# Optimization experiments

Hardware: AMD Instinct MI355X
Metric: run time of the kernel (lower is better)

## Reference

```python
import jax, jax.numpy as jnp
import numpy as np

HIDDEN = 1024
HEADS = 16
D_K = HIDDEN // HEADS
B, S = 2, 2048


def setup_inputs() -> dict:
    key = jax.random.key(0)
    ks = jax.random.split(key, 11)
    sc = 1.0 / np.sqrt(HIDDEN)
    return {
        "query": jax.random.normal(ks[0], (B, S, HIDDEN), jnp.float32),
        "key": jax.random.normal(ks[1], (B, S, HIDDEN), jnp.float32),
        "value": jax.random.normal(ks[2], (B, S, HIDDEN), jnp.float32),
        "w_q": jax.random.normal(ks[3], (HIDDEN, HIDDEN), jnp.float32) * sc,
        "b_q": jax.random.normal(ks[4], (HIDDEN,), jnp.float32) * 0.02,
        "w_k": jax.random.normal(ks[5], (HIDDEN, HIDDEN), jnp.float32) * sc,
        "b_k": jax.random.normal(ks[6], (HIDDEN,), jnp.float32) * 0.02,
        "w_v": jax.random.normal(ks[7], (HIDDEN, HIDDEN), jnp.float32) * sc,
        "b_v": jax.random.normal(ks[8], (HIDDEN,), jnp.float32) * 0.02,
        "w_o": jax.random.normal(ks[9], (HIDDEN, HIDDEN), jnp.float32) * sc,
        "b_o": jax.random.normal(ks[10], (HIDDEN,), jnp.float32) * 0.02,
    }


def reference(query, key, value, w_q, b_q, w_k, b_k, w_v, b_v, w_o, b_o):
    b, s, _ = query.shape
    # linear projections (torch Linear: x @ W^T + b)
    q = query @ w_q.T + b_q
    k = key @ w_k.T + b_k
    v = value @ w_v.T + b_v
    # [B, H, S, D]
    q = q.reshape(b, s, HEADS, D_K).transpose(0, 2, 1, 3)
    k = k.reshape(b, s, HEADS, D_K).transpose(0, 2, 1, 3)
    v = v.reshape(b, s, HEADS, D_K).transpose(0, 2, 1, 3)
    scale = jnp.float32(1.0 / np.sqrt(D_K))
    scores = jnp.einsum('bhqd,bhkd->bhqk', q, k) * scale  # [B,H,S,S]
    probs = jax.nn.softmax(scores, axis=-1)
    y = jnp.einsum('bhqk,bhkd->bhqd', probs, v)
    y = y.transpose(0, 2, 1, 3).reshape(b, s, HIDDEN)
    return y @ w_o.T + b_o
```

## Files before the change

kernel.cpp:

```cpp
#include <hip/hip_runtime.h>
#include <hip/hip_bf16.h>
#include <math.h>

#define HIDDEN 1024
#define HEADS 16
#define DK 64
#define BB 2
#define SS 2048
#define MROWS (BB*SS)

typedef __attribute__((ext_vector_type(8))) short short8;
typedef __attribute__((ext_vector_type(4))) float f32x4;
typedef __attribute__((ext_vector_type(16))) float f32x16;
typedef __attribute__((ext_vector_type(4))) unsigned short ushort4_t;

static __device__ __forceinline__ unsigned short f2bf(float f) {
    unsigned int u = __float_as_uint(f);
    u += 0x7fffu + ((u >> 16) & 1u);
    return (unsigned short)(u >> 16);
}

static __device__ __forceinline__ unsigned int cvtpk(float lo, float hi) {
    unsigned int r;
    asm volatile("v_cvt_pk_bf16_f32 %0, %1, %2" : "=v"(r) : "v"(lo), "v"(hi));
    return r;
}
static __device__ __forceinline__ void swap32(unsigned int& a, unsigned int& b) {
    asm volatile("v_permlane32_swap_b32 %0, %1" : "+v"(a), "+v"(b));
}

__global__ __launch_bounds__(256) void cast_all(
    const float* __restrict__ q, const float* __restrict__ k, const float* __restrict__ v,
    const float* __restrict__ wq, const float* __restrict__ wk, const float* __restrict__ wv,
    unsigned short* __restrict__ Xq, unsigned short* __restrict__ Xk, unsigned short* __restrict__ Xv,
    unsigned short* __restrict__ Wq, unsigned short* __restrict__ Wk, unsigned short* __restrict__ Wv) {
    int i = blockIdx.x * 256 + threadIdx.x;
    const float* src; unsigned short* dst; int off;
    if (i < (3 << 20)) {
        int w = i >> 20; off = i & ((1 << 20) - 1);
        src = (w == 0) ? q : (w == 1) ? k : v;
        dst = (w == 0) ? Xq : (w == 1) ? Xk : Xv;
    } else {
        int j = i - (3 << 20);
        int w = j >> 18; off = j & ((1 << 18) - 1);
        src = (w == 0) ? wq : (w == 1) ? wk : wv;
        dst = (w == 0) ? Wq : (w == 1) ? Wk : Wv;
    }
    float4 f = reinterpret_cast<const float4*>(src)[off];
    ushort4_t o;
    o.x = f2bf(f.x); o.y = f2bf(f.y); o.z = f2bf(f.z); o.w = f2bf(f.w);
    reinterpret_cast<ushort4_t*>(dst)[off] = o;
}

__global__ __launch_bounds__(256, 3) void gemm_qkv(
    const unsigned short* __restrict__ Xq, const unsigned short* __restrict__ Xk, const unsigned short* __restrict__ Xv,
    const unsigned short* __restrict__ Wq, const unsigned short* __restrict__ Wk, const unsigned short* __restrict__ Wv,
    const float* __restrict__ bq, const float* __restrict__ bk, const float* __restrict__ bv,
    unsigned short* __restrict__ Qb, unsigned short* __restrict__ Kb, unsigned short* __restrict__ Vt,
    float scale_q) {
    __shared__ unsigned short As[128][40];
    __shared__ unsigned short Bs[128][40];
    const int lid = blockIdx.x + 8 * (blockIdx.y + 32 * blockIdx.z);
    const int c = lid & 7, i2 = lid >> 3;
    const int nb = i2 & 7;
    const int band = c * 12 + (i2 >> 3);
    const int yb = band & 31;
    const int z  = band >> 5;
    const unsigned short* A  = (z == 0) ? Xq : (z == 1) ? Xk : Xv;
    const unsigned short* Wt = (z == 0) ? Wq : (z == 1) ? Wk : Wv;
    const float* bias = (z == 0) ? bq : (z == 1) ? bk : bv;
    unsigned short* O = (z == 0) ? Qb : (z == 1) ? Kb : Vt;
    const float oscale = (z == 0) ? scale_q : 1.0f;

    const int t    = threadIdx.x;
    const int lane = t & 63;
    const int wave = t >> 6;
    const int m0 = yb * 128;
    const int n0 = nb * 128;
    const int row  = t >> 2;
    const int col8 = (t & 3) * 8;

    const int wm = (wave >> 1) * 64;
    const int wn = (wave & 1) * 64;
    const int lr = lane & 15;
    const int lk = (lane >> 4) * 8;

    f32x4 acc[4][4];
#pragma unroll
    for (int i = 0; i < 4; i++)
#pragma unroll
        for (int j = 0; j < 4; j++) acc[i][j] = f32x4{0.f, 0.f, 0.f, 0.f};

    for (int k0 = 0; k0 < HIDDEN; k0 += 32) {
        short8 av0 = *reinterpret_cast<const short8*>(A  + (size_t)(m0 + row)      * HIDDEN + k0 + col8);
        short8 av1 = *reinterpret_cast<const short8*>(A  + (size_t)(m0 + row + 64) * HIDDEN + k0 + col8);
        short8 bv0 = *reinterpret_cast<const short8*>(Wt + (size_t)(n0 + row)      * HIDDEN + k0 + col8);
        short8 bv1 = *reinterpret_cast<const short8*>(Wt + (size_t)(n0 + row + 64) * HIDDEN + k0 + col8);
        __syncthreads();
        *reinterpret_cast<short8*>(&As[row][col8])      = av0;
        *reinterpret_cast<short8*>(&As[row + 64][col8]) = av1;
        *reinterpret_cast<short8*>(&Bs[row][col8])      = bv0;
        *reinterpret_cast<short8*>(&Bs[row + 64][col8]) = bv1;
        __syncthreads();
        short8 af[4], bfr[4];
#pragma unroll
        for (int i = 0; i < 4; i++) af[i]  = *reinterpret_cast<const short8*>(&As[wm + i * 16 + lr][lk]);
#pragma unroll
        for (int j = 0; j < 4; j++) bfr[j] = *reinterpret_cast<const short8*>(&Bs[wn + j * 16 + lr][lk]);
#pragma unroll
        for (int i = 0; i < 4; i++)
#pragma unroll
            for (int j = 0; j < 4; j++)
                acc[i][j] = __builtin_amdgcn_mfma_f32_16x16x32_bf16(af[i], bfr[j], acc[i][j], 0, 0, 0);
    }

#pragma unroll
    for (int i = 0; i < 4; i++) {
        int mrow = m0 + wm + i * 16 + (lane >> 4) * 4;
#pragma unroll
        for (int j = 0; j < 4; j++) {
            int ncol = n0 + wn + j * 16 + lr;
            float bvv = bias[ncol];
            int b_ = mrow >> 11;
            int h_ = ncol >> 6;
            int d_ = ncol & 63;
            if (z != 2) {
#pragma unroll
                for (int r = 0; r < 4; r++) {
                    int s_ = (mrow + r) & 2047;
                    O[(((size_t)(b_ * HEADS + h_)) * SS + s_) * DK + d_] = f2bf((acc[i][j][r] + bvv) * oscale);
                }
            } else {
                int s0 = mrow & 2047;
                ushort4_t pk;
                pk.x = f2bf(acc[i][j][0] + bvv);
                pk.y = f2bf(acc[i][j][1] + bvv);
                pk.z = f2bf(acc[i][j][2] + bvv);
                pk.w = f2bf(acc[i][j][3] + bvv);
                *reinterpret_cast<ushort4_t*>(O + (((size_t)(b_ * HEADS + h_) * DK + d_) * SS + s0)) = pk;
            }
        }
    }
}

__global__ __launch_bounds__(256) void gemm_o(const unsigned short* __restrict__ A,
                                              const float* __restrict__ Wt,
                                              const float* __restrict__ bias,
                                              float* __restrict__ O) {
    __shared__ unsigned short As[128][40];
    __shared__ unsigned short Bs[64][40];
    const int lid = blockIdx.x + 16 * blockIdx.y;
    const int c = lid & 7, i2 = lid >> 3;
    const int nb = i2 & 15;
    const int band = c * 4 + (i2 >> 4);
    const int t    = threadIdx.x;
    const int lane = t & 63;
    const int wave = t >> 6;
    const int m0 = band * 128;
    const int n0 = nb * 64;
    const int row  = t >> 2;
    const int col8 = (t & 3) * 8;

    const int wm = wave * 32;
    const int lr = lane & 15;
    const int lk = (lane >> 4) * 8;

    f32x4 acc[2][4];
#pragma unroll
    for (int i = 0; i < 2; i++)
#pragma unroll
        for (int j = 0; j < 4; j++) acc[i][j] = f32x4{0.f, 0.f, 0.f, 0.f};

    for (int k0 = 0; k0 < HIDDEN; k0 += 32) {
        short8 av0 = *reinterpret_cast<const short8*>(A + (size_t)(m0 + row)      * HIDDEN + k0 + col8);
        short8 av1 = *reinterpret_cast<const short8*>(A + (size_t)(m0 + row + 64) * HIDDEN + k0 + col8);
        const float* w0 = Wt + (size_t)(n0 + row) * HIDDEN + k0 + col8;
        float4 w00 = reinterpret_cast<const float4*>(w0)[0];
        float4 w01 = reinterpret_cast<const float4*>(w0)[1];
        __syncthreads();
        *reinterpret_cast<short8*>(&As[row][col8])      = av0;
        *reinterpret_cast<short8*>(&As[row + 64][col8]) = av1;
        {
            union { unsigned int u[4]; short8 s; } pk;
            pk.u[0] = cvtpk(w00.x, w00.y);
            pk.u[1] = cvtpk(w00.z, w00.w);
            pk.u[2] = cvtpk(w01.x, w01.y);
            pk.u[3] = cvtpk(w01.z, w01.w);
            *reinterpret_cast<short8*>(&Bs[row][col8]) = pk.s;
        }
        __syncthreads();
        short8 af[2], bfr[4];
#pragma unroll
        for (int i = 0; i < 2; i++) af[i]  = *reinterpret_cast<const short8*>(&As[wm + i * 16 + lr][lk]);
#pragma unroll
        for (int j = 0; j < 4; j++) bfr[j] = *reinterpret_cast<const short8*>(&Bs[j * 16 + lr][lk]);
#pragma unroll
        for (int i = 0; i < 2; i++)
#pragma unroll
            for (int j = 0; j < 4; j++)
                acc[i][j] = __builtin_amdgcn_mfma_f32_16x16x32_bf16(af[i], bfr[j], acc[i][j], 0, 0, 0);
    }

#pragma unroll
    for (int i = 0; i < 2; i++) {
        int mrow = m0 + wm + i * 16 + (lane >> 4) * 4;
#pragma unroll
        for (int j = 0; j < 4; j++) {
            int ncol = n0 + j * 16 + lr;
            float bvv = bias[ncol];
#pragma unroll
            for (int r = 0; r < 4; r++)
                O[(size_t)(mrow + r) * HIDDEN + ncol] = acc[i][j][r] + bvv;
        }
    }
}

__global__ __launch_bounds__(256, 2) void attn_kernel(const unsigned short* __restrict__ Qb,
                                                      const unsigned short* __restrict__ Kb,
                                                      const unsigned short* __restrict__ Vt,
                                                      unsigned short* __restrict__ Yb) {
    __shared__ __attribute__((aligned(16))) unsigned short Ksh[2][64 * 64];
    __shared__ __attribute__((aligned(16))) unsigned short Vsh[2][64 * 64];
    __shared__ float Lsh[4][32];

    const int t    = threadIdx.x;
    const int lane = t & 63;
    const int wave = t >> 6;
    const int fid  = blockIdx.x;
    const int qblk = (fid >> 3) & 15;
    const int bh   = (fid & 7) * 4 + (fid >> 7);
    const int b_ = bh >> 4, h_ = bh & 15;
    const int qbase = qblk * 128 + wave * 32;
    const unsigned short* Qp = Qb + (size_t)bh * SS * DK;
    const unsigned short* Kp = Kb + (size_t)bh * SS * DK;
    const unsigned short* Vp = Vt + (size_t)bh * DK * SS;
    const int lq = lane & 31;
    const int hi = lane >> 5;
    const int sr = lane >> 3;
    const int cs = (lane & 7) ^ sr;

    short8 qf[4];
#pragma unroll
    for (int c = 0; c < 4; c++)
        qf[c] = *reinterpret_cast<const short8*>(Qp + (size_t)(qbase + lq) * DK + c * 16 + hi * 8);

    f32x16 acc0 = {0.f}, acc1 = {0.f};
#pragma unroll
    for (int r = 0; r < 16; r++) { acc0[r] = 0.f; acc1[r] = 0.f; }
    float mi = -INFINITY, li = 0.f;

#define STAGE(BUF, KV0) do {                                                                 \
    __builtin_amdgcn_global_load_lds(                                                        \
        (const __attribute__((address_space(1))) unsigned int*)(Kp + (size_t)((KV0) + wave * 16 + sr) * DK + cs * 8), \
        (__attribute__((address_space(3))) unsigned int*)&Ksh[BUF][(wave * 16) * 64], 16, 0, 0); \
    __builtin_amdgcn_global_load_lds(                                                        \
        (const __attribute__((address_space(1))) unsigned int*)(Kp + (size_t)((KV0) + wave * 16 + 8 + sr) * DK + cs * 8), \
        (__attribute__((address_space(3))) unsigned int*)&Ksh[BUF][(wave * 16 + 8) * 64], 16, 0, 0); \
    __builtin_amdgcn_global_load_lds(                                                        \
        (const __attribute__((address_space(1))) unsigned int*)(Vp + (size_t)(wave * 16 + sr) * SS + (KV0) + cs * 8), \
        (__attribute__((address_space(3))) unsigned int*)&Vsh[BUF][(wave * 16) * 64], 16, 0, 0); \
    __builtin_amdgcn_global_load_lds(                                                        \
        (const __attribute__((address_space(1))) unsigned int*)(Vp + (size_t)(wave * 16 + 8 + sr) * SS + (KV0) + cs * 8), \
        (__attribute__((address_space(3))) unsigned int*)&Vsh[BUF][(wave * 16 + 8) * 64], 16, 0, 0); \
} while (0)

    STAGE(0, 0);
    __syncthreads();

    for (int kv0 = 0; kv0 < SS; kv0 += 64) {
        const int cur = (kv0 >> 6) & 1;
        if (kv0 + 64 < SS) STAGE(cur ^ 1, kv0 + 64);

        f32x16 sv0, sv1;
#pragma unroll
        for (int r = 0; r < 16; r++) { sv0[r] = 0.f; sv1[r] = 0.f; }
#pragma unroll
        for (int c = 0; c < 4; c++) {
            short8 kf0 = *reinterpret_cast<const short8*>(
                &Ksh[cur][lq * 64 + (((2 * c + hi) ^ (lq & 7)) << 3)]);
            short8 kf1 = *reinterpret_cast<const short8*>(
                &Ksh[cur][(32 + lq) * 64 + (((2 * c + hi) ^ (lq & 7)) << 3)]);
            sv0 = __builtin_amdgcn_mfma_f32_32x32x16_bf16(kf0, qf[c], sv0, 0, 0, 0);
            sv1 = __builtin_amdgcn_mfma_f32_32x32x16_bf16(kf1, qf[c], sv1, 0, 0, 0);
        }

        float vmax = sv0[0];
#pragma unroll
        for (int r = 0; r < 16; r++) { vmax = fmaxf(vmax, sv0[r]); vmax = fmaxf(vmax, sv1[r]); }
        vmax = fmaxf(vmax, __shfl_xor(vmax, 32));
        if (!__all(vmax <= mi + 8.0f)) {
            float mnew = fmaxf(mi, vmax);
            float sc = __builtin_amdgcn_exp2f(mi - mnew);
            li *= sc;
            acc0 = acc0 * sc;
            acc1 = acc1 * sc;
            mi = mnew;
        }
        float pt[2][16];
        float rs = 0.f;
#pragma unroll
        for (int r = 0; r < 16; r++) {
            pt[0][r] = __builtin_amdgcn_exp2f(sv0[r] - mi);
            pt[1][r] = __builtin_amdgcn_exp2f(sv1[r] - mi);
            rs += pt[0][r] + pt[1][r];
        }
        rs += __shfl_xor(rs, 32);
        li += rs;

        short8 fragP[4];
#pragma unroll
        for (int tt = 0; tt < 2; tt++)
#pragma unroll
            for (int cl = 0; cl < 2; cl++) {
                unsigned int w0 = cvtpk(pt[tt][cl * 8 + 0], pt[tt][cl * 8 + 1]);
                unsigned int w1 = cvtpk(pt[tt][cl * 8 + 2], pt[tt][cl * 8 + 3]);
                unsigned int w2 = cvtpk(pt[tt][cl * 8 + 4], pt[tt][cl * 8 + 5]);
                unsigned int w3 = cvtpk(pt[tt][cl * 8 + 6], pt[tt][cl * 8 + 7]);
                swap32(w0, w2);
                swap32(w1, w3);
                union { unsigned int u[4]; short8 s; } f;
                f.u[0] = w0; f.u[1] = w1; f.u[2] = w2; f.u[3] = w3;
                fragP[tt * 2 + cl] = f.s;
            }

#pragma unroll
        for (int cc = 0; cc < 4; cc++) {
            short8 vf0 = *reinterpret_cast<const short8*>(
                &Vsh[cur][lq * 64 + (((2 * cc + hi) ^ (lq & 7)) << 3)]);
            short8 vf1 = *reinterpret_cast<const short8*>(
                &Vsh[cur][(32 + lq) * 64 + (((2 * cc + hi) ^ (lq & 7)) << 3)]);
            acc0 = __builtin_amdgcn_mfma_f32_32x32x16_bf16(fragP[cc], vf0, acc0, 0, 0, 0);
            acc1 = __builtin_amdgcn_mfma_f32_32x32x16_bf16(fragP[cc], vf1, acc1, 0, 0, 0);
        }
        __syncthreads();
    }
#undef STAGE

    if (lane < 32) Lsh[wave][lq] = 1.0f / li;
    __syncthreads();
#pragma unroll
    for (int r = 0; r < 16; r++) {
        int qr = (r & 3) + 8 * (r >> 2) + 4 * hi;
        float inv = Lsh[wave][qr];
        size_t base = ((size_t)b_ * SS + qbase + qr) * HIDDEN + h_ * 64 + lq;
        Yb[base]      = f2bf(acc0[r] * inv);
        Yb[base + 32] = f2bf(acc1[r] * inv);
    }
}

extern "C" void kernel_launch(void* const* d_in, const int* in_sizes, int n_in,
                              void* d_out, int out_size, void* d_ws, size_t ws_size,
                              hipStream_t stream) {
    const float* query = (const float*)d_in[0];
    const float* key_  = (const float*)d_in[1];
    const float* value = (const float*)d_in[2];
    const float* w_q = (const float*)d_in[3];
    const float* b_q = (const float*)d_in[4];
    const float* w_k = (const float*)d_in[5];
    const float* b_k = (const float*)d_in[6];
    const float* w_v = (const float*)d_in[7];
    const float* b_v = (const float*)d_in[8];
    const float* w_o = (const float*)d_in[9];
    const float* b_o = (const float*)d_in[10];

    const size_t SZ_X = (size_t)MROWS * HIDDEN * 2;
    const size_t SZ_W = (size_t)HIDDEN * HIDDEN * 2;
    char* ws = (char*)d_ws;
    unsigned short* Xq = (unsigned short*)(ws);
    unsigned short* Xk = (unsigned short*)(ws + SZ_X);
    unsigned short* Xv = (unsigned short*)(ws + 2 * SZ_X);
    unsigned short* Wq = (unsigned short*)(ws + 3 * SZ_X);
    unsigned short* Wk = (unsigned short*)(ws + 3 * SZ_X + SZ_W);
    unsigned short* Wv = (unsigned short*)(ws + 3 * SZ_X + 2 * SZ_W);
    unsigned short* Qb  = (unsigned short*)(ws + 3 * SZ_X + 3 * SZ_W);
    unsigned short* Kbf = (unsigned short*)(ws + 4 * SZ_X + 3 * SZ_W);
    unsigned short* Vt  = (unsigned short*)(ws + 5 * SZ_X + 3 * SZ_W);
    unsigned short* Yb  = (unsigned short*)(ws + 6 * SZ_X + 3 * SZ_W);

    cast_all<<<15360, 256, 0, stream>>>(query, key_, value, w_q, w_k, w_v,
                                        Xq, Xk, Xv, Wq, Wk, Wv);

    const float SCALE_Q = 0.125f * 1.4426950408889634f;
    gemm_qkv<<<dim3(8, 32, 3), 256, 0, stream>>>(
        Xq, Xk, Xv, Wq, Wk, Wv, b_q, b_k, b_v, Qb, Kbf, Vt, SCALE_Q);

    attn_kernel<<<dim3(512), 256, 0, stream>>>(Qb, Kbf, Vt, Yb);

    gemm_o<<<dim3(16, 32), 256, 0, stream>>>(Yb, w_o, b_o, (float*)d_out);
}
```

Baseline: 132.3 us.

## Fuse fp32 casts into QKV GEMM and split attention KV into two halves

```diff
diff --git a/kernel.cpp b/kernel.cpp
--- a/kernel.cpp
+++ b/kernel.cpp
@@ -19,6 +19,9 @@
     u += 0x7fffu + ((u >> 16) & 1u);
     return (unsigned short)(u >> 16);
 }
+static __device__ __forceinline__ float bf2f(unsigned short s) {
+    return __uint_as_float(((unsigned int)s) << 16);
+}
 
 static __device__ __forceinline__ unsigned int cvtpk(float lo, float hi) {
     unsigned int r;
@@ -28,33 +31,18 @@
 static __device__ __forceinline__ void swap32(unsigned int& a, unsigned int& b) {
     asm volatile("v_permlane32_swap_b32 %0, %1" : "+v"(a), "+v"(b));
 }
-
-__global__ __launch_bounds__(256) void cast_all(
-    const float* __restrict__ q, const float* __restrict__ k, const float* __restrict__ v,
-    const float* __restrict__ wq, const float* __restrict__ wk, const float* __restrict__ wv,
-    unsigned short* __restrict__ Xq, unsigned short* __restrict__ Xk, unsigned short* __restrict__ Xv,
-    unsigned short* __restrict__ Wq, unsigned short* __restrict__ Wk, unsigned short* __restrict__ Wv) {
-    int i = blockIdx.x * 256 + threadIdx.x;
-    const float* src; unsigned short* dst; int off;
-    if (i < (3 << 20)) {
-        int w = i >> 20; off = i & ((1 << 20) - 1);
-        src = (w == 0) ? q : (w == 1) ? k : v;
-        dst = (w == 0) ? Xq : (w == 1) ? Xk : Xv;
-    } else {
-        int j = i - (3 << 20);
-        int w = j >> 18; off = j & ((1 << 18) - 1);
-        src = (w == 0) ? wq : (w == 1) ? wk : wv;
-        dst = (w == 0) ? Wq : (w == 1) ? Wk : Wv;
-    }
-    float4 f = reinterpret_cast<const float4*>(src)[off];
-    ushort4_t o;
-    o.x = f2bf(f.x); o.y = f2bf(f.y); o.z = f2bf(f.z); o.w = f2bf(f.w);
-    reinterpret_cast<ushort4_t*>(dst)[off] = o;
+static __device__ __forceinline__ short8 pack_bf16x8(float4 lo, float4 hi) {
+    union { unsigned int u[4]; short8 s; } r;
+    r.u[0] = cvtpk(lo.x, lo.y);
+    r.u[1] = cvtpk(lo.z, lo.w);
+    r.u[2] = cvtpk(hi.x, hi.y);
+    r.u[3] = cvtpk(hi.z, hi.w);
+    return r.s;
 }
 
 __global__ __launch_bounds__(256, 3) void gemm_qkv(
-    const unsigned short* __restrict__ Xq, const unsigned short* __restrict__ Xk, const unsigned short* __restrict__ Xv,
-    const unsigned short* __restrict__ Wq, const unsigned short* __restrict__ Wk, const unsigned short* __restrict__ Wv,
+    const float* __restrict__ Xq, const float* __restrict__ Xk, const float* __restrict__ Xv,
+    const float* __restrict__ Wq, const float* __restrict__ Wk, const float* __restrict__ Wv,
     const float* __restrict__ bq, const float* __restrict__ bk, const float* __restrict__ bv,
     unsigned short* __restrict__ Qb, unsigned short* __restrict__ Kb, unsigned short* __restrict__ Vt,
     float scale_q) {
@@ -66,8 +54,8 @@
     const int band = c * 12 + (i2 >> 3);
     const int yb = band & 31;
     const int z  = band >> 5;
-    const unsigned short* A  = (z == 0) ? Xq : (z == 1) ? Xk : Xv;
-    const unsigned short* Wt = (z == 0) ? Wq : (z == 1) ? Wk : Wv;
+    const float* A  = (z == 0) ? Xq : (z == 1) ? Xk : Xv;
+    const float* Wt = (z == 0) ? Wq : (z == 1) ? Wk : Wv;
     const float* bias = (z == 0) ? bq : (z == 1) ? bk : bv;
     unsigned short* O = (z == 0) ? Qb : (z == 1) ? Kb : Vt;
     const float oscale = (z == 0) ? scale_q : 1.0f;
@@ -92,15 +80,23 @@
         for (int j = 0; j < 4; j++) acc[i][j] = f32x4{0.f, 0.f, 0.f, 0.f};
 
     for (int k0 = 0; k0 < HIDDEN; k0 += 32) {
-        short8 av0 = *reinterpret_cast<const short8*>(A  + (size_t)(m0 + row)      * HIDDEN + k0 + col8);
-        short8 av1 = *reinterpret_cast<const short8*>(A  + (size_t)(m0 + row + 64) * HIDDEN + k0 + col8);
-        short8 bv0 = *reinterpret_cast<const short8*>(Wt + (size_t)(n0 + row)      * HIDDEN + k0 + col8);
-        short8 bv1 = *reinterpret_cast<const short8*>(Wt + (size_t)(n0 + row + 64) * HIDDEN + k0 + col8);
+        const float* a0 = A  + (size_t)(m0 + row)      * HIDDEN + k0 + col8;
+        const float* a1 = A  + (size_t)(m0 + row + 64) * HIDDEN + k0 + col8;
+        const float* w0 = Wt + (size_t)(n0 + row)      * HIDDEN + k0 + col8;
+        const float* w1 = Wt + (size_t)(n0 + row + 64) * HIDDEN + k0 + col8;
+        float4 a00 = reinterpret_cast<const float4*>(a0)[0];
+        float4 a01 = reinterpret_cast<const float4*>(a0)[1];
+        float4 a10 = reinterpret_cast<const float4*>(a1)[0];
+        float4 a11 = reinterpret_cast<const float4*>(a1)[1];
+        float4 w00 = reinterpret_cast<const float4*>(w0)[0];
+        float4 w01 = reinterpret_cast<const float4*>(w0)[1];
+        float4 w10 = reinterpret_cast<const float4*>(w1)[0];
+        float4 w11 = reinterpret_cast<const float4*>(w1)[1];
         __syncthreads();
-        *reinterpret_cast<short8*>(&As[row][col8])      = av0;
-        *reinterpret_cast<short8*>(&As[row + 64][col8]) = av1;
-        *reinterpret_cast<short8*>(&Bs[row][col8])      = bv0;
-        *reinterpret_cast<short8*>(&Bs[row + 64][col8]) = bv1;
+        *reinterpret_cast<short8*>(&As[row][col8])      = pack_bf16x8(a00, a01);
+        *reinterpret_cast<short8*>(&As[row + 64][col8]) = pack_bf16x8(a10, a11);
+        *reinterpret_cast<short8*>(&Bs[row][col8])      = pack_bf16x8(w00, w01);
+        *reinterpret_cast<short8*>(&Bs[row + 64][col8]) = pack_bf16x8(w10, w11);
         __syncthreads();
         short8 af[4], bfr[4];
 #pragma unroll
@@ -180,14 +176,7 @@
         __syncthreads();
         *reinterpret_cast<short8*>(&As[row][col8])      = av0;
         *reinterpret_cast<short8*>(&As[row + 64][col8]) = av1;
-        {
-            union { unsigned int u[4]; short8 s; } pk;
-            pk.u[0] = cvtpk(w00.x, w00.y);
-            pk.u[1] = cvtpk(w00.z, w00.w);
-            pk.u[2] = cvtpk(w01.x, w01.y);
-            pk.u[3] = cvtpk(w01.z, w01.w);
-            *reinterpret_cast<short8*>(&Bs[row][col8]) = pk.s;
-        }
+        *reinterpret_cast<short8*>(&Bs[row][col8])      = pack_bf16x8(w00, w01);
         __syncthreads();
         short8 af[2], bfr[4];
 #pragma unroll
@@ -215,10 +204,12 @@
     }
 }
 
-__global__ __launch_bounds__(256, 2) void attn_kernel(const unsigned short* __restrict__ Qb,
+__global__ __launch_bounds__(256, 4) void attn_kernel(const unsigned short* __restrict__ Qb,
                                                       const unsigned short* __restrict__ Kb,
                                                       const unsigned short* __restrict__ Vt,
-                                                      unsigned short* __restrict__ Yb) {
+                                                      unsigned short* __restrict__ Yb0,
+                                                      unsigned short* __restrict__ Yb1,
+                                                      float2* __restrict__ ml) {
     __shared__ __attribute__((aligned(16))) unsigned short Ksh[2][64 * 64];
     __shared__ __attribute__((aligned(16))) unsigned short Vsh[2][64 * 64];
     __shared__ float Lsh[4][32];
@@ -227,10 +218,15 @@
     const int lane = t & 63;
     const int wave = t >> 6;
     const int fid  = blockIdx.x;
-    const int qblk = (fid >> 3) & 15;
-    const int bh   = (fid & 7) * 4 + (fid >> 7);
+    const int c    = fid & 7;
+    const int i    = fid >> 3;
+    const int qblk = i & 15;
+    const int pair = c * 8 + (i >> 4);
+    const int bh   = pair >> 1;
+    const int kvh  = pair & 1;
     const int b_ = bh >> 4, h_ = bh & 15;
     const int qbase = qblk * 128 + wave * 32;
+    const int kvbase = kvh << 10;
     const unsigned short* Qp = Qb + (size_t)bh * SS * DK;
     const unsigned short* Kp = Kb + (size_t)bh * SS * DK;
     const unsigned short* Vp = Vt + (size_t)bh * DK * SS;
@@ -241,10 +237,10 @@
 
     short8 qf[4];
 #pragma unroll
-    for (int c = 0; c < 4; c++)
-        qf[c] = *reinterpret_cast<const short8*>(Qp + (size_t)(qbase + lq) * DK + c * 16 + hi * 8);
-
-    f32x16 acc0 = {0.f}, acc1 = {0.f};
+    for (int cc = 0; cc < 4; cc++)
+        qf[cc] = *reinterpret_cast<const short8*>(Qp + (size_t)(qbase + lq) * DK + cc * 16 + hi * 8);
+
+    f32x16 acc0, acc1;
 #pragma unroll
     for (int r = 0; r < 16; r++) { acc0[r] = 0.f; acc1[r] = 0.f; }
     float mi = -INFINITY, li = 0.f;
@@ -264,24 +260,24 @@
         (__attribute__((address_space(3))) unsigned int*)&Vsh[BUF][(wave * 16 + 8) * 64], 16, 0, 0); \
 } while (0)
 
-    STAGE(0, 0);
+    STAGE(0, kvbase);
     __syncthreads();
 
-    for (int kv0 = 0; kv0 < SS; kv0 += 64) {
+    for (int kv0 = kvbase; kv0 < kvbase + 1024; kv0 += 64) {
         const int cur = (kv0 >> 6) & 1;
-        if (kv0 + 64 < SS) STAGE(cur ^ 1, kv0 + 64);
+        if (kv0 + 64 < kvbase + 1024) STAGE(cur ^ 1, kv0 + 64);
 
         f32x16 sv0, sv1;
 #pragma unroll
         for (int r = 0; r < 16; r++) { sv0[r] = 0.f; sv1[r] = 0.f; }
 #pragma unroll
-        for (int c = 0; c < 4; c++) {
+        for (int cc = 0; cc < 4; cc++) {
             short8 kf0 = *reinterpret_cast<const short8*>(
-                &Ksh[cur][lq * 64 + (((2 * c + hi) ^ (lq & 7)) << 3)]);
+                &Ksh[cur][lq * 64 + (((2 * cc + hi) ^ (lq & 7)) << 3)]);
             short8 kf1 = *reinterpret_cast<const short8*>(
-                &Ksh[cur][(32 + lq) * 64 + (((2 * c + hi) ^ (lq & 7)) << 3)]);
-            sv0 = __builtin_amdgcn_mfma_f32_32x32x16_bf16(kf0, qf[c], sv0, 0, 0, 0);
-            sv1 = __builtin_amdgcn_mfma_f32_32x32x16_bf16(kf1, qf[c], sv1, 0, 0, 0);
+                &Ksh[cur][(32 + lq) * 64 + (((2 * cc + hi) ^ (lq & 7)) << 3)]);
+            sv0 = __builtin_amdgcn_mfma_f32_32x32x16_bf16(kf0, qf[cc], sv0, 0, 0, 0);
+            sv1 = __builtin_amdgcn_mfma_f32_32x32x16_bf16(kf1, qf[cc], sv1, 0, 0, 0);
         }
 
         float vmax = sv0[0];
@@ -336,16 +332,49 @@
     }
 #undef STAGE
 
-    if (lane < 32) Lsh[wave][lq] = 1.0f / li;
+    unsigned short* Yp = kvh ? Yb1 : Yb0;
+    if (lane < 32) {
+        Lsh[wave][lq] = 1.0f / li;
+        ml[(((size_t)kvh * 32 + bh) << 11) + qbase + lq] = float2{mi, li};
+    }
     __syncthreads();
 #pragma unroll
     for (int r = 0; r < 16; r++) {
         int qr = (r & 3) + 8 * (r >> 2) + 4 * hi;
         float inv = Lsh[wave][qr];
         size_t base = ((size_t)b_ * SS + qbase + qr) * HIDDEN + h_ * 64 + lq;
-        Yb[base]      = f2bf(acc0[r] * inv);
-        Yb[base + 32] = f2bf(acc1[r] * inv);
-    }
+        Yp[base]      = f2bf(acc0[r] * inv);
+        Yp[base + 32] = f2bf(acc1[r] * inv);
+    }
+}
+
+__global__ __launch_bounds__(256) void combine_halves(const unsigned short* __restrict__ Yb0,
+                                                      const unsigned short* __restrict__ Yb1,
+                                                      const float2* __restrict__ ml,
+                                                      unsigned short* __restrict__ Yb) {
+    int j = blockIdx.x * 256 + threadIdx.x;
+    int chunk = j & 127;
+    int s = (j >> 7) & 2047;
+    int b = j >> 18;
+    int h = chunk >> 3;
+    int bh = b * 16 + h;
+    float2 m0 = ml[((size_t)bh << 11) + s];
+    float2 m1 = ml[(((size_t)32 + bh) << 11) + s];
+    float M = fmaxf(m0.x, m1.x);
+    float l0 = m0.y * __builtin_amdgcn_exp2f(m0.x - M);
+    float l1 = m1.y * __builtin_amdgcn_exp2f(m1.x - M);
+    float inv = 1.0f / (l0 + l1);
+    float w0 = l0 * inv, w1 = l1 * inv;
+    short8 a = reinterpret_cast<const short8*>(Yb0)[j];
+    short8 bb = reinterpret_cast<const short8*>(Yb1)[j];
+    union { unsigned int u[4]; short8 s8; } o;
+#pragma unroll
+    for (int k = 0; k < 4; k++) {
+        float lo = w0 * bf2f((unsigned short)a[2 * k])     + w1 * bf2f((unsigned short)bb[2 * k]);
+        float hi = w0 * bf2f((unsigned short)a[2 * k + 1]) + w1 * bf2f((unsigned short)bb[2 * k + 1]);
+        o.u[k] = cvtpk(lo, hi);
+    }
+    reinterpret_cast<short8*>(Yb)[j] = o.s8;
 }
 
 extern "C" void kernel_launch(void* const* d_in, const int* in_sizes, int n_in,
@@ -364,27 +393,22 @@
     const float* b_o = (const float*)d_in[10];
 
     const size_t SZ_X = (size_t)MROWS * HIDDEN * 2;
-    const size_t SZ_W = (size_t)HIDDEN * HIDDEN * 2;
     char* ws = (char*)d_ws;
-    unsigned short* Xq = (unsigned short*)(ws);
-    unsigned short* Xk = (unsigned short*)(ws + SZ_X);
-    unsigned short* Xv = (unsigned short*)(ws + 2 * SZ_X);
-    unsigned short* Wq = (unsigned short*)(ws + 3 * SZ_X);
-    unsigned short* Wk = (unsigned short*)(ws + 3 * SZ_X + SZ_W);
-    unsigned short* Wv = (unsigned short*)(ws + 3 * SZ_X + 2 * SZ_W);
-    unsigned short* Qb  = (unsigned short*)(ws + 3 * SZ_X + 3 * SZ_W);
-    unsigned short* Kbf = (unsigned short*)(ws + 4 * SZ_X + 3 * SZ_W);
-    unsigned short* Vt  = (unsigned short*)(ws + 5 * SZ_X + 3 * SZ_W);
-    unsigned short* Yb  = (unsigned short*)(ws + 6 * SZ_X + 3 * SZ_W);
-
-    cast_all<<<15360, 256, 0, stream>>>(query, key_, value, w_q, w_k, w_v,
-                                        Xq, Xk, Xv, Wq, Wk, Wv);
+    unsigned short* Qb  = (unsigned short*)(ws);
+    unsigned short* Kbf = (unsigned short*)(ws + SZ_X);
+    unsigned short* Vt  = (unsigned short*)(ws + 2 * SZ_X);
+    unsigned short* Yb0 = (unsigned short*)(ws + 3 * SZ_X);
+    unsigned short* Yb1 = (unsigned short*)(ws + 4 * SZ_X);
+    unsigned short* Yb  = (unsigned short*)(ws + 5 * SZ_X);
+    float2*         ml  = (float2*)(ws + 6 * SZ_X);
 
     const float SCALE_Q = 0.125f * 1.4426950408889634f;
     gemm_qkv<<<dim3(8, 32, 3), 256, 0, stream>>>(
-        Xq, Xk, Xv, Wq, Wk, Wv, b_q, b_k, b_v, Qb, Kbf, Vt, SCALE_Q);
-
-    attn_kernel<<<dim3(512), 256, 0, stream>>>(Qb, Kbf, Vt, Yb);
+        query, key_, value, w_q, w_k, w_v, b_q, b_k, b_v, Qb, Kbf, Vt, SCALE_Q);
+
+    attn_kernel<<<dim3(1024), 256, 0, stream>>>(Qb, Kbf, Vt, Yb0, Yb1, ml);
+
+    combine_halves<<<dim3(2048), 256, 0, stream>>>(Yb0, Yb1, ml, Yb);
 
     gemm_o<<<dim3(16, 32), 256, 0, stream>>>(Yb, w_o, b_o, (float*)d_out);
 }
```

New measurement: 129.1 us. -2.4%, faster.
